# Performance work log

Hardware: AMD Instinct MI355X
Metric: run time of the kernel (lower is better)

The kernel has to match this reference:

```python
import jax, jax.numpy as jnp
import numpy as np

B, N = 8, 512
C_IN, C_E, C_MID, C_OUT = 64, 16, 64, 64


def _linear_params(key, fan_in, fan_out):
    k1, k2 = jax.random.split(key)
    bound = 1.0 / np.sqrt(fan_in)
    W = jax.random.uniform(k1, (fan_out, fan_in), jnp.float32, -bound, bound)
    b = jax.random.uniform(k2, (fan_out,), jnp.float32, -bound, bound)
    return W, b


def setup_inputs() -> dict:
    key = jax.random.key(0)
    ks = jax.random.split(key, 9)
    x = jax.random.normal(ks[0], (B, N, C_IN), jnp.float32)
    adj = jax.random.randint(ks[1], (B, N, N), 0, 2).astype(jnp.float32)
    edge_attr = jax.random.normal(ks[2], (B, N, N, C_E), jnp.float32)
    W1, b1 = _linear_params(ks[3], C_IN, C_MID)
    W2, b2 = _linear_params(ks[4], C_IN, C_MID)
    We, be = _linear_params(ks[5], C_E, C_MID)
    Wn, bn = _linear_params(ks[6], C_MID, C_MID)   # user-supplied net: Linear(mid, mid)
    Wo1, bo1 = _linear_params(ks[7], C_IN, C_OUT)
    Wo2, bo2 = _linear_params(ks[8], C_MID, C_OUT)
    return {"x": x, "adj": adj, "edge_attr": edge_attr,
            "W1": W1, "b1": b1, "W2": W2, "b2": b2, "We": We, "be": be,
            "Wn": Wn, "bn": bn, "Wo1": Wo1, "bo1": bo1, "Wo2": Wo2, "bo2": bo2}


def reference(x, adj, edge_attr, W1, b1, W2, b2, We, be, Wn, bn, Wo1, bo1, Wo2, bo2):
    # node / edge projections
    msg_1 = jnp.einsum('bnc,mc->bnm', x, W1) + b1          # [B, N, mid]
    msg_2 = jnp.einsum('bnc,mc->bnm', x, W2) + b2          # [B, N, mid]
    msg_e = jnp.einsum('bijc,mc->bijm', edge_attr, We) + be  # [B, N, N, mid]
    # broadcast sum: msg_1 over dim 1, msg_2 over dim 2 (matches torch unsqueeze)
    msg = msg_1[:, None, :, :] + msg_2[:, :, None, :] + msg_e  # [B, N, N, mid]
    # net applied after hard-coded relu
    msg = jnp.einsum('bijm,km->bijk', jax.nn.relu(msg), Wn) + bn
    # sum aggregator with adjacency mask, reduced over dim 1
    msg = jnp.einsum('bijm,bij->bjm', msg, adj)            # [B, N, mid]
    h_1 = jnp.einsum('bnc,oc->bno', x, Wo1) + bo1
    h_2 = jnp.einsum('bnm,om->bno', msg, Wo2) + bo2
    return h_1 + h_2
```

## Files before the change

### kernel.cpp

```cpp
#include <hip/hip_runtime.h>
#include <stdint.h>

#define B_   8
#define N_   512
#define CE_  16
#define BN_  (B_*N_)
#define Q_   8

typedef __attribute__((ext_vector_type(8))) short bf16x8;
typedef __attribute__((ext_vector_type(4))) short bf16x4;
typedef __attribute__((ext_vector_type(4))) float f32x4;
typedef __attribute__((ext_vector_type(2))) float f32x2;
typedef __attribute__((ext_vector_type(4))) int   i32x4;
typedef __attribute__((ext_vector_type(2))) int   i32x2;

#if defined(__has_builtin)
#  if __has_builtin(__builtin_amdgcn_mfma_f32_16x16x16bf16_1k)
#    define HAVE_MFMA16 1
#  endif
#endif
#ifndef HAVE_MFMA16
#  define HAVE_MFMA16 0
#endif

union PackA8 { i32x4 i; bf16x8 h; };
union PackA4 { i32x2 i; bf16x4 h; };
union V4     { f32x4 v; f32x2 h[2]; };

__device__ __forceinline__ unsigned short f2bf_rne(float f) {
  unsigned u = __float_as_uint(f);
  u += 0x7FFFu + ((u >> 16) & 1u);
  return (unsigned short)(u >> 16);
}

__device__ __forceinline__ f32x2 pk_fma(f32x2 a, f32x2 b, f32x2 c) {
  f32x2 d;
  asm("v_pk_fma_f32 %0, %1, %2, %3" : "=v"(d) : "v"(a), "v"(b), "v"(c));
  return d;
}
__device__ __forceinline__ f32x2 pk_add2(f32x2 a, f32x2 b) {
  f32x2 d;
  asm("v_pk_add_f32 %0, %1, %2" : "=v"(d) : "v"(a), "v"(b));
  return d;
}

__global__ __launch_bounds__(256) void k1_pre(
    const float* __restrict__ x,
    const float* __restrict__ W1,  const float* __restrict__ b1,
    const float* __restrict__ W2,  const float* __restrict__ b2,
    const float* __restrict__ Wn,  const float* __restrict__ bn,
    const float* __restrict__ Wo1, const float* __restrict__ bo1,
    const float* __restrict__ Wo2, const float* __restrict__ bo2,
    const float* __restrict__ We,
    float* __restrict__ m1, float* __restrict__ m2, float* __restrict__ base,
    float* __restrict__ Wc, float* __restrict__ bc, unsigned* __restrict__ wePack)
{
  const int tid = threadIdx.x;
  const int bx  = blockIdx.x;
  if (bx >= BN_/4) {
    const int q4 = bx - BN_/4;
    for (int idx = tid; idx < 16*64; idx += 256) {
      const int k = q4*16 + (idx >> 6), m = idx & 63;
      float acc = 0.f;
      #pragma unroll 8
      for (int t = 0; t < 64; ++t) acc += Wo2[k*64 + t] * Wn[t*64 + m];
      Wc[k*64 + m] = acc;
    }
    if (q4 == 0) {
      if (tid < 64) {
        float acc = 0.f;
        for (int t = 0; t < 64; ++t) acc += Wo2[tid*64 + t] * bn[t];
        bc[tid] = acc;
      }
      const int c = tid >> 6, lane = tid & 63, col = lane & 15, quad = lane >> 4;
#if HAVE_MFMA16
      const float* wr = We + (c*16 + col)*CE_ + quad*4;
      wePack[tid*2+0] = ((unsigned)f2bf_rne(wr[1]) << 16) | f2bf_rne(wr[0]);
      wePack[tid*2+1] = ((unsigned)f2bf_rne(wr[3]) << 16) | f2bf_rne(wr[2]);
#else
      unsigned p0=0, p1=0, p2=0, p3=0;
      if (quad < 2) {
        const float* wr = We + (c*16 + col)*CE_ + quad*8;
        p0 = ((unsigned)f2bf_rne(wr[1]) << 16) | f2bf_rne(wr[0]);
        p1 = ((unsigned)f2bf_rne(wr[3]) << 16) | f2bf_rne(wr[2]);
        p2 = ((unsigned)f2bf_rne(wr[5]) << 16) | f2bf_rne(wr[4]);
        p3 = ((unsigned)f2bf_rne(wr[7]) << 16) | f2bf_rne(wr[6]);
      }
      wePack[tid*4+0]=p0; wePack[tid*4+1]=p1; wePack[tid*4+2]=p2; wePack[tid*4+3]=p3;
#endif
    }
    return;
  }
  const int r = tid >> 6, m = tid & 63;
  const int row = bx*4 + r;
  __shared__ float xs[4][64];
  xs[r][m] = x[(size_t)row*64 + m];
  __syncthreads();
  const float* xr = xs[r];
  float a1 = b1[m], a2 = b2[m], a3 = bo1[m] + bo2[m];
  const float* w1r = W1  + m*64;
  const float* w2r = W2  + m*64;
  const float* w3r = Wo1 + m*64;
  #pragma unroll 8
  for (int c = 0; c < 64; ++c) {
    const float xv = xr[c];
    a1 += xv * w1r[c];
    a2 += xv * w2r[c];
    a3 += xv * w3r[c];
  }
  m1[(size_t)row*64 + m]   = a1;
  m2[(size_t)row*64 + m]   = a2;
  base[(size_t)row*64 + m] = a3;
}

__global__ __launch_bounds__(256) void k2_main(
    const float* __restrict__ edge, const float* __restrict__ adj,
    const unsigned* __restrict__ wePack, const float* __restrict__ be,
    const float* __restrict__ m1,   const float* __restrict__ m2,
    float* __restrict__ pS, float* __restrict__ pdeg)
{
  const int tid  = threadIdx.x;
  const int lane = tid & 63;
  const int wid  = tid >> 6;
  const int col  = lane & 15;
  const int quad = lane >> 4;

  const int blk = blockIdx.x;
  const int q   = blk & 7;
  const int grp = blk >> 3;
  const int b   = grp >> 5;
  const int j0  = (grp & 31) << 4;
  const int i0  = q*64 + wid*16;

#if HAVE_MFMA16
  bf16x4 bfr[4];
  { const i32x2* wp = (const i32x2*)wePack;
    #pragma unroll
    for (int c = 0; c < 4; ++c) { PackA4 u; u.i = wp[c*64 + lane]; bfr[c] = u.h; } }
#else
  bf16x8 bfr[4];
  { const i32x4* wp = (const i32x4*)wePack;
    #pragma unroll
    for (int c = 0; c < 4; ++c) { PackA8 u; u.i = wp[c*64 + lane]; bfr[c] = u.h; } }
#endif

  f32x4 m1f[4];
  #pragma unroll
  for (int c = 0; c < 4; ++c) {
    const float bev = be[c*16 + col];
    const float* mp = m1 + (size_t)(b*N_ + j0 + quad*4)*64 + c*16 + col;
    m1f[c].x = mp[0]   + bev;
    m1f[c].y = mp[64]  + bev;
    m1f[c].z = mp[128] + bev;
    m1f[c].w = mp[192] + bev;
  }

  const f32x2 z2 = {0.f, 0.f};
  f32x2 S2[4][2];
  #pragma unroll
  for (int c = 0; c < 4; ++c) { S2[c][0] = z2; S2[c][1] = z2; }
  f32x2 dg0 = z2, dg1 = z2;

#if HAVE_MFMA16
  const float* ep = edge + ((size_t)(b*N_ + i0)*N_ + (j0 + col))*CE_ + quad*4;
#else
  const float* ep = edge + ((size_t)(b*N_ + i0)*N_ + (j0 + col))*CE_ + (quad & 1)*8;
#endif
  const float* ap  = adj + (size_t)(b*N_ + i0)*N_ + j0 + quad*4;
  const float* m2p = m2  + (size_t)(b*N_ + i0)*64 + col;

  for (int it = 0; it < 16; ++it) {
#if HAVE_MFMA16
    const f32x4 e0 = *(const f32x4*)ep;
    PackA4 ua;
    ua.i.x = (int)__builtin_amdgcn_perm(__float_as_uint(e0.y), __float_as_uint(e0.x), 0x07060302u);
    ua.i.y = (int)__builtin_amdgcn_perm(__float_as_uint(e0.w), __float_as_uint(e0.z), 0x07060302u);
#else
    const f32x4 e0 = *(const f32x4*)(ep);
    const f32x4 e1 = *(const f32x4*)(ep + 4);
    PackA8 ua;
    ua.i.x = (int)__builtin_amdgcn_perm(__float_as_uint(e0.y), __float_as_uint(e0.x), 0x07060302u);
    ua.i.y = (int)__builtin_amdgcn_perm(__float_as_uint(e0.w), __float_as_uint(e0.z), 0x07060302u);
    ua.i.z = (int)__builtin_amdgcn_perm(__float_as_uint(e1.y), __float_as_uint(e1.x), 0x07060302u);
    ua.i.w = (int)__builtin_amdgcn_perm(__float_as_uint(e1.w), __float_as_uint(e1.z), 0x07060302u);
#endif
    V4 av; av.v = *(const f32x4*)ap;

    #pragma unroll
    for (int c = 0; c < 4; ++c) {
      const float m2v = m2p[c*16];
      f32x4 cin;
      cin.x = m1f[c].x + m2v;
      cin.y = m1f[c].y + m2v;
      cin.z = m1f[c].z + m2v;
      cin.w = m1f[c].w + m2v;
#if HAVE_MFMA16
      f32x4 r = __builtin_amdgcn_mfma_f32_16x16x16bf16_1k(ua.h, bfr[c], cin, 0, 0, 0);
#else
      f32x4 r = __builtin_amdgcn_mfma_f32_16x16x32_bf16(ua.h, bfr[c], cin, 0, 0, 0);
#endif
      r.x = fmaxf(r.x, 0.f);
      r.y = fmaxf(r.y, 0.f);
      r.z = fmaxf(r.z, 0.f);
      r.w = fmaxf(r.w, 0.f);
      V4 rv; rv.v = r;
      S2[c][0] = pk_fma(av.h[0], rv.h[0], S2[c][0]);
      S2[c][1] = pk_fma(av.h[1], rv.h[1], S2[c][1]);
    }
    dg0 = pk_add2(dg0, av.h[0]);
    dg1 = pk_add2(dg1, av.h[1]);
    ep  += N_ * CE_;
    ap  += N_;
    m2p += 64;
  }

  __shared__ float red[4][16*68];
  __shared__ float redd[4][16];
  #pragma unroll
  for (int c = 0; c < 4; ++c) {
    red[wid][(quad*4 + 0)*68 + c*16 + col] = S2[c][0].x;
    red[wid][(quad*4 + 1)*68 + c*16 + col] = S2[c][0].y;
    red[wid][(quad*4 + 2)*68 + c*16 + col] = S2[c][1].x;
    red[wid][(quad*4 + 3)*68 + c*16 + col] = S2[c][1].y;
  }
  if (col == 0) {
    redd[wid][quad*4 + 0] = dg0.x;
    redd[wid][quad*4 + 1] = dg0.y;
    redd[wid][quad*4 + 2] = dg1.x;
    redd[wid][quad*4 + 3] = dg1.y;
  }
  __syncthreads();

  float* oS = pS + ((size_t)q*BN_ + b*N_ + j0)*64;
  #pragma unroll
  for (int t = 0; t < 4; ++t) {
    const int idx = t*256 + tid;
    const int row = idx >> 6, ch = idx & 63;
    oS[idx] = red[0][row*68 + ch] + red[1][row*68 + ch]
            + red[2][row*68 + ch] + red[3][row*68 + ch];
  }
  if (tid < 16) {
    pdeg[(size_t)q*BN_ + b*N_ + j0 + tid] =
      redd[0][tid] + redd[1][tid] + redd[2][tid] + redd[3][tid];
  }
}

__global__ __launch_bounds__(256) void k3_out(
    const float* __restrict__ pS, const float* __restrict__ pdeg,
    const float* __restrict__ base, const float* __restrict__ Wc,
    const float* __restrict__ bc, float* __restrict__ out)
{
  const int tid = threadIdx.x;
  const int r   = tid >> 6;
  const int k   = tid & 63;
  const int row = blockIdx.x*4 + r;
  __shared__ float sm[4][64];
  float s = 0.f, dr = 0.f;
  #pragma unroll
  for (int q = 0; q < Q_; ++q) {
    s  += pS[((size_t)q*BN_ + row)*64 + k];
    dr += pdeg[(size_t)q*BN_ + row];
  }
  sm[r][k] = s;
  __syncthreads();
  float acc = base[(size_t)row*64 + k] + dr * bc[k];
  const float* wr  = Wc + k*64;
  const float* smr = sm[r];
  #pragma unroll
  for (int m = 0; m < 64; ++m) acc += smr[m] * wr[m];
  out[(size_t)row*64 + k] = acc;
}

extern "C" void kernel_launch(void* const* d_in, const int* in_sizes, int n_in,
                              void* d_out, int out_size, void* d_ws, size_t ws_size,
                              hipStream_t stream)
{
  const float* x    = (const float*)d_in[0];
  const float* adj  = (const float*)d_in[1];
  const float* edge = (const float*)d_in[2];
  const float* W1   = (const float*)d_in[3];
  const float* b1   = (const float*)d_in[4];
  const float* W2   = (const float*)d_in[5];
  const float* b2   = (const float*)d_in[6];
  const float* We   = (const float*)d_in[7];
  const float* be   = (const float*)d_in[8];
  const float* Wn   = (const float*)d_in[9];
  const float* bn   = (const float*)d_in[10];
  const float* Wo1  = (const float*)d_in[11];
  const float* bo1  = (const float*)d_in[12];
  const float* Wo2  = (const float*)d_in[13];
  const float* bo2  = (const float*)d_in[14];
  float* out = (float*)d_out;

  char* ws = (char*)d_ws;
  float* m1   = (float*)(ws);
  float* m2   = (float*)(ws + (size_t)(1u<<20));
  float* base = (float*)(ws + (size_t)2*(1u<<20));
  float* Wc   = (float*)(ws + (size_t)3*(1u<<20));
  float* bc   = (float*)(ws + (size_t)3*(1u<<20) + 16384);
  float* pdeg = (float*)(ws + (size_t)3*(1u<<20) + 17408);
  float* pS   = (float*)(ws + (size_t)3*(1u<<20) + 17408 + 131072);
  unsigned* wePack = (unsigned*)(ws + (size_t)3*(1u<<20) + 17408 + 131072
                                 + (size_t)Q_*BN_*64*4);

  k1_pre<<<BN_/4 + 4, 256, 0, stream>>>(x, W1, b1, W2, b2, Wn, bn,
                                        Wo1, bo1, Wo2, bo2, We,
                                        m1, m2, base, Wc, bc, wePack);
  k2_main<<<2048, 256, 0, stream>>>(edge, adj, wePack, be, m1, m2, pS, pdeg);
  k3_out<<<BN_/4, 256, 0, stream>>>(pS, pdeg, base, Wc, bc, out);
}
```

Measured before the change: 270.7 us.

## Transpose m2 for vector loads, nontemporal edge loads, remap block order

Stores m2 in an interleaved layout so each lane fetches its four per-channel values with a single 16-byte load instead of four scalar loads. Edge and adjacency streams use nontemporal loads to keep them from polluting cache. The k2 block index mapping is swapped so consecutive blocks share the same i-chunk q, and k3's row order is permuted, both aimed at cache and XCD locality. These add layout coupling between kernels and depend on how the hardware schedules blocks.

```diff
diff --git a/kernel.cpp b/kernel.cpp
--- a/kernel.cpp
+++ b/kernel.cpp
@@ -52,7 +52,7 @@
     const float* __restrict__ Wo1, const float* __restrict__ bo1,
     const float* __restrict__ Wo2, const float* __restrict__ bo2,
     const float* __restrict__ We,
-    float* __restrict__ m1, float* __restrict__ m2, float* __restrict__ base,
+    float* __restrict__ m1, float* __restrict__ m2t, float* __restrict__ base,
     float* __restrict__ Wc, float* __restrict__ bc, unsigned* __restrict__ wePack)
 {
   const int tid = threadIdx.x;
@@ -108,15 +108,15 @@
     a2 += xv * w2r[c];
     a3 += xv * w3r[c];
   }
-  m1[(size_t)row*64 + m]   = a1;
-  m2[(size_t)row*64 + m]   = a2;
-  base[(size_t)row*64 + m] = a3;
+  m1[(size_t)row*64 + m]                       = a1;
+  m2t[(size_t)row*64 + (m & 15)*4 + (m >> 4)]  = a2;
+  base[(size_t)row*64 + m]                     = a3;
 }
 
 __global__ __launch_bounds__(256) void k2_main(
     const float* __restrict__ edge, const float* __restrict__ adj,
     const unsigned* __restrict__ wePack, const float* __restrict__ be,
-    const float* __restrict__ m1,   const float* __restrict__ m2,
+    const float* __restrict__ m1,   const float* __restrict__ m2t,
     float* __restrict__ pS, float* __restrict__ pdeg)
 {
   const int tid  = threadIdx.x;
@@ -126,8 +126,8 @@
   const int quad = lane >> 4;
 
   const int blk = blockIdx.x;
-  const int q   = blk & 7;
-  const int grp = blk >> 3;
+  const int q   = blk >> 8;
+  const int grp = blk & 255;
   const int b   = grp >> 5;
   const int j0  = (grp & 31) << 4;
   const int i0  = q*64 + wid*16;
@@ -167,28 +167,29 @@
   const float* ep = edge + ((size_t)(b*N_ + i0)*N_ + (j0 + col))*CE_ + (quad & 1)*8;
 #endif
   const float* ap  = adj + (size_t)(b*N_ + i0)*N_ + j0 + quad*4;
-  const float* m2p = m2  + (size_t)(b*N_ + i0)*64 + col;
+  const float* m2p = m2t + (size_t)(b*N_ + i0)*64 + col*4;
 
   for (int it = 0; it < 16; ++it) {
 #if HAVE_MFMA16
-    const f32x4 e0 = *(const f32x4*)ep;
+    const f32x4 e0 = __builtin_nontemporal_load((const f32x4*)ep);
     PackA4 ua;
     ua.i.x = (int)__builtin_amdgcn_perm(__float_as_uint(e0.y), __float_as_uint(e0.x), 0x07060302u);
     ua.i.y = (int)__builtin_amdgcn_perm(__float_as_uint(e0.w), __float_as_uint(e0.z), 0x07060302u);
 #else
-    const f32x4 e0 = *(const f32x4*)(ep);
-    const f32x4 e1 = *(const f32x4*)(ep + 4);
+    const f32x4 e0 = __builtin_nontemporal_load((const f32x4*)(ep));
+    const f32x4 e1 = __builtin_nontemporal_load((const f32x4*)(ep + 4));
     PackA8 ua;
     ua.i.x = (int)__builtin_amdgcn_perm(__float_as_uint(e0.y), __float_as_uint(e0.x), 0x07060302u);
     ua.i.y = (int)__builtin_amdgcn_perm(__float_as_uint(e0.w), __float_as_uint(e0.z), 0x07060302u);
     ua.i.z = (int)__builtin_amdgcn_perm(__float_as_uint(e1.y), __float_as_uint(e1.x), 0x07060302u);
     ua.i.w = (int)__builtin_amdgcn_perm(__float_as_uint(e1.w), __float_as_uint(e1.z), 0x07060302u);
 #endif
-    V4 av; av.v = *(const f32x4*)ap;
+    V4 av; av.v = __builtin_nontemporal_load((const f32x4*)ap);
+    const f32x4 m2q = *(const f32x4*)m2p;
 
     #pragma unroll
     for (int c = 0; c < 4; ++c) {
-      const float m2v = m2p[c*16];
+      const float m2v = (c == 0) ? m2q.x : (c == 1) ? m2q.y : (c == 2) ? m2q.z : m2q.w;
       f32x4 cin;
       cin.x = m1f[c].x + m2v;
       cin.y = m1f[c].y + m2v;
@@ -253,7 +254,11 @@
   const int tid = threadIdx.x;
   const int r   = tid >> 6;
   const int k   = tid & 63;
-  const int row = blockIdx.x*4 + r;
+  const int bid = blockIdx.x;
+  const int x8  = bid & 7;
+  const int u   = bid >> 3;
+  const int g   = x8 + 8*(u >> 2);
+  const int row = g*16 + (u & 3)*4 + r;
   __shared__ float sm[4][64];
   float s = 0.f, dr = 0.f;
   #pragma unroll
@@ -294,7 +299,7 @@
 
   char* ws = (char*)d_ws;
   float* m1   = (float*)(ws);
-  float* m2   = (float*)(ws + (size_t)(1u<<20));
+  float* m2t  = (float*)(ws + (size_t)(1u<<20));
   float* base = (float*)(ws + (size_t)2*(1u<<20));
   float* Wc   = (float*)(ws + (size_t)3*(1u<<20));
   float* bc   = (float*)(ws + (size_t)3*(1u<<20) + 16384);
@@ -305,7 +310,7 @@
 
   k1_pre<<<BN_/4 + 4, 256, 0, stream>>>(x, W1, b1, W2, b2, Wn, bn,
                                         Wo1, bo1, Wo2, bo2, We,
-                                        m1, m2, base, Wc, bc, wePack);
-  k2_main<<<2048, 256, 0, stream>>>(edge, adj, wePack, be, m1, m2, pS, pdeg);
+                                        m1, m2t, base, Wc, bc, wePack);
+  k2_main<<<2048, 256, 0, stream>>>(edge, adj, wePack, be, m1, m2t, pS, pdeg);
   k3_out<<<BN_/4, 256, 0, stream>>>(pS, pdeg, base, Wc, bc, out);
 }
```

Measured after the change: 269.2 us. About the same (-0.6%).
